# Kernel tuning notes

Hardware: AMD Instinct MI355X
Metric: run time of the kernel (lower is better)

Reference implementation:

```python
import jax, jax.numpy as jnp
import numpy as np

K = 3        # kernel size
STRIDE = 1
PAD = 1
DIL = 1


def setup_inputs() -> dict:
    key = jax.random.key(0)
    k1, k2, k3 = jax.random.split(key, 3)
    B, C, H, W, O = 4, 256, 64, 64, 256
    x = jax.random.normal(k1, (B, C, H, W), jnp.float32)
    # offset/mask predictor conv (kaiming-ish small init, zero bias per module init)
    w_off = jax.random.normal(k2, (3 * K * K, C, K, K), jnp.float32) * 0.01
    b_off = jnp.zeros((3 * K * K,), jnp.float32)
    # modulated deformable conv weight (bias=False)
    w_conv = jax.random.normal(k3, (O, C, K, K), jnp.float32) * 0.05
    return {"x": x, "w_off": w_off, "b_off": b_off, "w_conv": w_conv}


def _dfconv(x, w_off, b_off, w_conv):
    B, C, H, W = x.shape
    KK = K * K
    # 1) standard conv predicting offsets+mask: [B, 3*K*K, Ho, Wo]
    om = jax.lax.conv_general_dilated(
        x, w_off, (STRIDE, STRIDE), [(PAD, PAD), (PAD, PAD)],
        rhs_dilation=(DIL, DIL), dimension_numbers=("NCHW", "OIHW", "NCHW"))
    om = om + b_off[None, :, None, None]
    offset = om[:, : 2 * KK]                      # (dy,dx) interleaved per tap
    mask = jax.nn.sigmoid(om[:, 2 * KK:])         # [B, KK, Ho, Wo]
    Ho, Wo = offset.shape[-2:]
    off = offset.reshape(B, KK, 2, Ho, Wo)
    dy, dx = off[:, :, 0], off[:, :, 1]           # [B, KK, Ho, Wo]

    # 2) per-tap sampling coordinates in input space
    ky = jnp.repeat(jnp.arange(K), K).astype(x.dtype)   # tap row index [KK]
    kx = jnp.tile(jnp.arange(K), K).astype(x.dtype)     # tap col index [KK]
    base_y = (jnp.arange(Ho) * STRIDE - PAD).astype(x.dtype)
    base_x = (jnp.arange(Wo) * STRIDE - PAD).astype(x.dtype)
    py = dy + base_y[None, None, :, None] + (ky * DIL)[None, :, None, None]
    px = dx + base_x[None, None, None, :] + (kx * DIL)[None, :, None, None]

    # 3) bilinear sample with zero padding outside the image
    y0f = jnp.floor(py)
    x0f = jnp.floor(px)
    wy = py - y0f
    wx = px - x0f
    y0 = y0f.astype(jnp.int32)
    x0 = x0f.astype(jnp.int32)
    img = x.reshape(B, C, H * W)

    def gather(yi, xi):
        valid = ((yi >= 0) & (yi < H) & (xi >= 0) & (xi < W)).astype(x.dtype)
        idx = jnp.clip(yi, 0, H - 1) * W + jnp.clip(xi, 0, W - 1)
        g = jnp.take_along_axis(img, idx.reshape(B, 1, -1), axis=2)
        return g.reshape(B, C, KK, Ho, Wo) * valid[:, None]

    wy_ = wy[:, None]  # [B,1,KK,Ho,Wo]
    wx_ = wx[:, None]
    val = (gather(y0, x0) * (1 - wy_) * (1 - wx_)
           + gather(y0, x0 + 1) * (1 - wy_) * wx_
           + gather(y0 + 1, x0) * wy_ * (1 - wx_)
           + gather(y0 + 1, x0 + 1) * wy_ * wx_)

    # 4) modulation + weighted accumulation over taps and channels
    val = val * mask[:, None]                      # [B,C,KK,Ho,Wo]
    out = jnp.einsum("bckhw,ock->bohw", val, w_conv.reshape(w_conv.shape[0], C, KK))
    return out


def reference(x, w_off, b_off, w_conv):
    return _dfconv(x, w_off, b_off, w_conv)
```

## Files before the change

### kernel.cpp

```cpp
#include <hip/hip_runtime.h>
#include <hip/hip_bf16.h>

#define XH   64
#define XW   64
#define CIN  256
#define COUT 256
#define BATCH 4
#define KK9  9
#define M_TOT 16384
#define K_TOT 2304
#define NKSTEP 36

typedef __attribute__((ext_vector_type(8))) short short8;
typedef __attribute__((ext_vector_type(4))) float f32x4;

#define XT_OFF   0
#define XT_BYTES (BATCH*4096*CIN*2)
#define WT_OFF   (XT_OFF + XT_BYTES)
#define WT_BYTES (COUT*K_TOT*2)
#define WOT_OFF  (WT_OFF + WT_BYTES)
#define WOT_BYTES (36*2*2*64*8*2)

__device__ __forceinline__ float b2f(short s) {
  union { float f; unsigned u; } x;
  x.u = ((unsigned)(unsigned short)s) << 16;
  return x.f;
}

struct Taps { short8 t00, t01, t10, t11; };

__global__ __launch_bounds__(256) void k0_wt(const float* __restrict__ wconv,
                                             __hip_bfloat16* __restrict__ Wt3) {
  int e = blockIdx.x * 256 + threadIdx.x;
  int j3   = e & 7;
  int lane = (e >> 3) & 63;
  int kc   = (e >> 9) & 1;
  int og   = (e >> 10) & 15;
  int tk   = e >> 14;
  int o = og * 16 + (lane & 15);
  int k = tk * 64 + kc * 32 + ((lane >> 4) << 3) + j3;
  int kk = k >> 8, c = k & 255;
  float v = wconv[(o * CIN + c) * KK9 + kk];
  Wt3[e] = __float2bfloat16(v);
}

__global__ __launch_bounds__(256) void k0b_wot(const float* __restrict__ woff,
                                               __hip_bfloat16* __restrict__ Wot3) {
  int e = blockIdx.x * 256 + threadIdx.x;
  int j3   = e & 7;
  int lane = (e >> 3) & 63;
  int kc   = (e >> 9) & 1;
  int wc   = (e >> 10) & 1;
  int tk   = e >> 11;
  int oc = wc * 16 + (lane & 15);
  int k = tk * 64 + kc * 32 + ((lane >> 4) << 3) + j3;
  int kk = k >> 8, c = k & 255;
  float v = (oc < 27) ? woff[((size_t)(oc * 256 + c)) * 9 + kk] : 0.f;
  Wot3[e] = __float2bfloat16(v);
}

__global__ __launch_bounds__(256) void kt_xt(const float* __restrict__ x,
                                             __hip_bfloat16* __restrict__ xTh) {
  __shared__ float t[64][65];
  int blk = blockIdx.x;
  int hwg = blk & 63;
  int cg  = (blk >> 6) & 3;
  int b   = blk >> 8;
  int hw0 = hwg * 64, c0 = cg * 64;
  int l = threadIdx.x & 63, q = threadIdx.x >> 6;
  const float* xb = x + ((size_t)(b * 256 + c0) << 12) + hw0;
#pragma unroll
  for (int i = 0; i < 16; ++i) {
    int cl = q * 16 + i;
    t[cl][l] = xb[((size_t)cl << 12) + l];
  }
  __syncthreads();
  __hip_bfloat16* xTb = xTh + (((size_t)b << 12) + hw0) * 256 + c0;
#pragma unroll
  for (int i = 0; i < 16; ++i) {
    int hwl = q * 16 + i;
    xTb[(size_t)hwl * 256 + l] = __float2bfloat16(t[l][hwl]);
  }
}

__global__ __launch_bounds__(256, 2) void k23_fused(const __hip_bfloat16* __restrict__ xTh,
                                                    const __hip_bfloat16* __restrict__ Wt3,
                                                    const __hip_bfloat16* __restrict__ Wot3,
                                                    const float* __restrict__ boff,
                                                    float* __restrict__ out) {
  __shared__ __align__(16) __hip_bfloat16 sPV[2][32 * 64];
  __shared__ float sOM[32][33];
  __shared__ float sw00[288], sw01[288], sw10[288], sw11[288];
  __shared__ int   so00[288], so01[288], so10[288], so11[288];

  int bid = blockIdx.x;
  int tm = ((bid & 7) << 6) | (bid >> 3);
  int tid = threadIdx.x;
  int wv = tid >> 6, lane = tid & 63;
  int lo = lane & 15, hi = lane >> 4;
  int b = tm >> 7;
  int m0 = tm * 32;

  {
    int wr = wv >> 1, wc = wv & 1;
    int prow = tid >> 3;
    int pkb  = (tid & 7) * 8;
    int pcolz = pkb ^ ((prow & 7) << 3);
    int m_s = m0 + prow;
    int hw_s = m_s & 4095, h_s = hw_s >> 6, w_s = hw_s & 63;

    auto loadPatch = [&](int tkq) -> short8 {
      int kk = tkq >> 2, cc = tkq & 3;
      int ky = kk / 3, kx = kk - ky * 3;
      int yy = h_s + ky - 1, xx = w_s + kx - 1;
      short8 h8 = {0, 0, 0, 0, 0, 0, 0, 0};
      if (((unsigned)yy < 64u) && ((unsigned)xx < 64u))
        h8 = *(const short8*)(xTh + ((((size_t)b << 12) + yy * 64 + xx) << 8) + cc * 64 + pkb);
      return h8;
    };
    auto loadWot = [&](int tkq, short8 (&w2)[2]) {
#pragma unroll
      for (int kc = 0; kc < 2; ++kc)
        w2[kc] = *(const short8*)((const char*)Wot3
                  + ((((size_t)tkq * 2 + wc) * 2 + kc) << 10) + lane * 16);
    };

    f32x4 acc1 = {0.f, 0.f, 0.f, 0.f};
    short8 PA, PB, wUA[2], wUB[2];
    PA = loadPatch(0);
    loadWot(0, wUA);
    *(short8*)&sPV[0][prow * 64 + pcolz] = PA;
    PB = loadPatch(1);
    asm volatile("s_waitcnt lgkmcnt(0)" ::: "memory");
    __builtin_amdgcn_s_barrier();

    auto p1body = [&](int tk, short8& Puse, short8& Pload,
                      short8 (&wU)[2], short8 (&wL)[2]) {
      int cb = tk & 1, nb = cb ^ 1;
      loadWot(min(tk + 1, NKSTEP - 1), wL);
      Pload = loadPatch(min(tk + 2, NKSTEP - 1));
      __builtin_amdgcn_sched_barrier(0);
      *(short8*)&sPV[nb][prow * 64 + pcolz] = Puse;
#pragma unroll
      for (int kc = 0; kc < 2; ++kc) {
        int cz = (kc * 32 + hi * 8) ^ ((lo & 7) << 3);
        short8 bfr = *(const short8*)&sPV[cb][(wr * 16 + lo) * 64 + cz];
        acc1 = __builtin_amdgcn_mfma_f32_16x16x32_bf16(wU[kc], bfr, acc1, 0, 0, 0);
      }
      if (tk + 1 < NKSTEP) {
        asm volatile("s_waitcnt lgkmcnt(0)" ::: "memory");
        __builtin_amdgcn_s_barrier();
      }
    };
    for (int tkp = 0; tkp < NKSTEP; tkp += 2) {
      p1body(tkp,     PB, PA, wUA, wUB);
      p1body(tkp + 1, PA, PB, wUB, wUA);
    }

    int oc0 = wc * 16 + hi * 4;
#pragma unroll
    for (int r = 0; r < 4; ++r) {
      float bias = (oc0 + r < 27) ? boff[oc0 + r] : 0.f;
      sOM[wr * 16 + lo][oc0 + r] = acc1[r] + bias;
    }
  }
  __syncthreads();

  for (int it = tid; it < 288; it += 256) {
    int kk = it >> 5, row = it & 31;
    int m = m0 + row;
    int hw = m & 4095, h = hw >> 6, w = hw & 63;
    float dy = sOM[row][2 * kk];
    float dx = sOM[row][2 * kk + 1];
    float mz = sOM[row][18 + kk];
    int ky = kk / 3, kx = kk - ky * 3;
    float py = dy + (float)(h - 1 + ky);
    float px = dx + (float)(w - 1 + kx);
    float y0f = floorf(py), x0f = floorf(px);
    float wy = py - y0f, wx = px - x0f;
    int y0 = (int)y0f, x0 = (int)x0f;
    bool vy0 = (unsigned)y0 < 64u, vy1 = (unsigned)(y0 + 1) < 64u;
    bool vx0 = (unsigned)x0 < 64u, vx1 = (unsigned)(x0 + 1) < 64u;
    int cy0 = min(max(y0, 0), 63), cy1 = min(max(y0 + 1, 0), 63);
    int cx0 = min(max(x0, 0), 63), cx1 = min(max(x0 + 1, 0), 63);
    float mask = 1.f / (1.f + __expf(-mz));
    sw00[it] = (vy0 && vx0) ? (1.f - wy) * (1.f - wx) * mask : 0.f;
    sw01[it] = (vy0 && vx1) ? (1.f - wy) * wx * mask : 0.f;
    sw10[it] = (vy1 && vx0) ? wy * (1.f - wx) * mask : 0.f;
    sw11[it] = (vy1 && vx1) ? wy * wx * mask : 0.f;
    so00[it] = cy0 * 64 + cx0;
    so01[it] = cy0 * 64 + cx1;
    so10[it] = cy1 * 64 + cx0;
    so11[it] = cy1 * 64 + cx1;
  }
  __syncthreads();

  const __hip_bfloat16* xb = xTh + ((size_t)b << 20);
  int vrow = tid >> 3;
  int chq  = tid & 7;
  int colz = (chq * 8) ^ ((vrow & 7) << 3);

  auto loadTaps = [&](int tkq, Taps& T) {
    int it = (tkq >> 2) * 32 + vrow;
    const __hip_bfloat16* base = xb + (tkq & 3) * 64 + chq * 8;
    T.t00 = *(const short8*)(base + (size_t)so00[it] * 256);
    T.t01 = *(const short8*)(base + (size_t)so01[it] * 256);
    T.t10 = *(const short8*)(base + (size_t)so10[it] * 256);
    T.t11 = *(const short8*)(base + (size_t)so11[it] * 256);
  };
  auto buildV = [&](int tkq, const Taps& T, int buf) {
    int it = (tkq >> 2) * 32 + vrow;
    float a00 = sw00[it], a01 = sw01[it], a10 = sw10[it], a11 = sw11[it];
    __hip_bfloat16 h8[8];
#pragma unroll
    for (int j = 0; j < 8; ++j) {
      float v = a00 * b2f(T.t00[j]) + a01 * b2f(T.t01[j])
              + a10 * b2f(T.t10[j]) + a11 * b2f(T.t11[j]);
      h8[j] = __float2bfloat16(v);
    }
    *(short8*)&sPV[buf][vrow * 64 + colz] = *(const short8*)h8;
  };
  auto loadW = [&](int tkq, short8 (&aw)[8]) {
#pragma unroll
    for (int fo = 0; fo < 4; ++fo)
#pragma unroll
      for (int kc = 0; kc < 2; ++kc)
        aw[fo * 2 + kc] = *(const short8*)((const char*)Wt3
                          + ((((size_t)tkq * 16 + (wv * 4 + fo)) * 2 + kc) << 10)
                          + lane * 16);
  };

  f32x4 zero4 = {0.f, 0.f, 0.f, 0.f};
  f32x4 acc[4][2];
#pragma unroll
  for (int fo = 0; fo < 4; ++fo)
#pragma unroll
    for (int fm = 0; fm < 2; ++fm) acc[fo][fm] = zero4;

  Taps TA, TB;
  short8 awA[8], awB[8];
  loadW(0, awA);
  loadTaps(0, TA);
  buildV(0, TA, 0);
  loadTaps(1, TB);
  asm volatile("s_waitcnt lgkmcnt(0)" ::: "memory");
  __builtin_amdgcn_s_barrier();

  auto body = [&](int tk, Taps& Tuse, Taps& Tload,
                  short8 (&awUse)[8], short8 (&awLoad)[8]) {
    int cb = tk & 1, nb = cb ^ 1;
    loadW(min(tk + 1, NKSTEP - 1), awLoad);
    loadTaps(min(tk + 2, NKSTEP - 1), Tload);
    __builtin_amdgcn_sched_barrier(0);
    buildV(min(tk + 1, NKSTEP - 1), Tuse, nb);

    __builtin_amdgcn_s_setprio(1);
#pragma unroll
    for (int kc = 0; kc < 2; ++kc) {
      int cz = (kc * 32 + hi * 8) ^ ((lo & 7) << 3);
      short8 bv[2];
#pragma unroll
      for (int fm = 0; fm < 2; ++fm)
        bv[fm] = *(const short8*)&sPV[cb][(fm * 16 + lo) * 64 + cz];
#pragma unroll
      for (int fo = 0; fo < 4; ++fo)
#pragma unroll
        for (int fm = 0; fm < 2; ++fm)
          acc[fo][fm] = __builtin_amdgcn_mfma_f32_16x16x32_bf16(awUse[fo * 2 + kc], bv[fm], acc[fo][fm], 0, 0, 0);
    }
    __builtin_amdgcn_s_setprio(0);

    if (tk + 1 < NKSTEP) {
      asm volatile("s_waitcnt lgkmcnt(0)" ::: "memory");
      __builtin_amdgcn_s_barrier();
    }
  };

  for (int tkp = 0; tkp < NKSTEP; tkp += 2) {
    body(tkp,     TB, TA, awA, awB);
    body(tkp + 1, TA, TB, awB, awA);
  }

  int hwbase = m0 & 4095;
#pragma unroll
  for (int fo = 0; fo < 4; ++fo) {
    int o = wv * 64 + fo * 16 + hi * 4;
#pragma unroll
    for (int fm = 0; fm < 2; ++fm) {
      int mloc = hwbase + fm * 16 + lo;
#pragma unroll
      for (int r = 0; r < 4; ++r)
        out[((size_t)(b * 256 + o + r)) * 4096 + mloc] = acc[fo][fm][r];
    }
  }
}

extern "C" void kernel_launch(void* const* d_in, const int* in_sizes, int n_in,
                              void* d_out, int out_size, void* d_ws, size_t ws_size,
                              hipStream_t stream) {
  (void)in_sizes; (void)n_in; (void)out_size; (void)ws_size;
  const float* x     = (const float*)d_in[0];
  const float* woff  = (const float*)d_in[1];
  const float* boff  = (const float*)d_in[2];
  const float* wconv = (const float*)d_in[3];
  char* ws = (char*)d_ws;
  __hip_bfloat16* xTh  = (__hip_bfloat16*)(ws + XT_OFF);
  __hip_bfloat16* Wt3  = (__hip_bfloat16*)(ws + WT_OFF);
  __hip_bfloat16* Wot3 = (__hip_bfloat16*)(ws + WOT_OFF);
  float* out = (float*)d_out;

  hipLaunchKernelGGL(k0_wt,     dim3(2304), dim3(256), 0, stream, wconv, Wt3);
  hipLaunchKernelGGL(k0b_wot,   dim3(288),  dim3(256), 0, stream, woff, Wot3);
  hipLaunchKernelGGL(kt_xt,     dim3(1024), dim3(256), 0, stream, x, xTh);
  hipLaunchKernelGGL(k23_fused, dim3(512),  dim3(256), 0, stream, xTh, Wt3, Wot3, boff, out);
}
```

Before: 71.13 us.

## Double fused kernel block size to 512 threads with split-K offset conv

Raises the fused kernel from 256 to 512 threads per block, each wave now owning 32 output channels instead of 64. The offset-conv phase is split across two 256-thread groups, each reducing half of K into its own partial buffer; the partials and bias are summed afterwards. The main loop's gather switches to 4-element loads per thread. This is meant to raise occupancy and spread the gather and MFMA work over more waves. The cost is that the offset-conv loop loses its software pipelining and now issues two full barriers per step.

```diff
diff --git a/kernel.cpp b/kernel.cpp
--- a/kernel.cpp
+++ b/kernel.cpp
@@ -10,8 +10,10 @@
 #define M_TOT 16384
 #define K_TOT 2304
 #define NKSTEP 36
+#define HKSTEP 18
 
 typedef __attribute__((ext_vector_type(8))) short short8;
+typedef __attribute__((ext_vector_type(4))) short short4v;
 typedef __attribute__((ext_vector_type(4))) float f32x4;
 
 #define XT_OFF   0
@@ -27,7 +29,7 @@
   return x.f;
 }
 
-struct Taps { short8 t00, t01, t10, t11; };
+struct Taps4 { short4v t00, t01, t10, t11; };
 
 __global__ __launch_bounds__(256) void k0_wt(const float* __restrict__ wconv,
                                              __hip_bfloat16* __restrict__ Wt3) {
@@ -83,13 +85,13 @@
   }
 }
 
-__global__ __launch_bounds__(256, 2) void k23_fused(const __hip_bfloat16* __restrict__ xTh,
+__global__ __launch_bounds__(512, 4) void k23_fused(const __hip_bfloat16* __restrict__ xTh,
                                                     const __hip_bfloat16* __restrict__ Wt3,
                                                     const __hip_bfloat16* __restrict__ Wot3,
                                                     const float* __restrict__ boff,
                                                     float* __restrict__ out) {
   __shared__ __align__(16) __hip_bfloat16 sPV[2][32 * 64];
-  __shared__ float sOM[32][33];
+  __shared__ float sOMp[2][32][33];
   __shared__ float sw00[288], sw01[288], sw10[288], sw11[288];
   __shared__ int   so00[288], so01[288], so10[288], so11[288];
 
@@ -102,77 +104,51 @@
   int m0 = tm * 32;
 
   {
-    int wr = wv >> 1, wc = wv & 1;
-    int prow = tid >> 3;
-    int pkb  = (tid & 7) * 8;
+    int g  = wv >> 2;
+    int wq = wv & 3;
+    int wr = wq >> 1, wc = wq & 1;
+    int gt = tid & 255;
+    int prow = gt >> 3;
+    int pkb  = (gt & 7) * 8;
     int pcolz = pkb ^ ((prow & 7) << 3);
     int m_s = m0 + prow;
     int hw_s = m_s & 4095, h_s = hw_s >> 6, w_s = hw_s & 63;
 
-    auto loadPatch = [&](int tkq) -> short8 {
-      int kk = tkq >> 2, cc = tkq & 3;
+    f32x4 acc1 = {0.f, 0.f, 0.f, 0.f};
+    for (int s = 0; s < HKSTEP; ++s) {
+      int tk = g * HKSTEP + s;
+      int kk = tk >> 2, cc = tk & 3;
       int ky = kk / 3, kx = kk - ky * 3;
       int yy = h_s + ky - 1, xx = w_s + kx - 1;
       short8 h8 = {0, 0, 0, 0, 0, 0, 0, 0};
       if (((unsigned)yy < 64u) && ((unsigned)xx < 64u))
         h8 = *(const short8*)(xTh + ((((size_t)b << 12) + yy * 64 + xx) << 8) + cc * 64 + pkb);
-      return h8;
-    };
-    auto loadWot = [&](int tkq, short8 (&w2)[2]) {
-#pragma unroll
-      for (int kc = 0; kc < 2; ++kc)
-        w2[kc] = *(const short8*)((const char*)Wot3
-                  + ((((size_t)tkq * 2 + wc) * 2 + kc) << 10) + lane * 16);
-    };
-
-    f32x4 acc1 = {0.f, 0.f, 0.f, 0.f};
-    short8 PA, PB, wUA[2], wUB[2];
-    PA = loadPatch(0);
-    loadWot(0, wUA);
-    *(short8*)&sPV[0][prow * 64 + pcolz] = PA;
-    PB = loadPatch(1);
-    asm volatile("s_waitcnt lgkmcnt(0)" ::: "memory");
-    __builtin_amdgcn_s_barrier();
-
-    auto p1body = [&](int tk, short8& Puse, short8& Pload,
-                      short8 (&wU)[2], short8 (&wL)[2]) {
-      int cb = tk & 1, nb = cb ^ 1;
-      loadWot(min(tk + 1, NKSTEP - 1), wL);
-      Pload = loadPatch(min(tk + 2, NKSTEP - 1));
-      __builtin_amdgcn_sched_barrier(0);
-      *(short8*)&sPV[nb][prow * 64 + pcolz] = Puse;
+      *(short8*)&sPV[g][prow * 64 + pcolz] = h8;
+      __syncthreads();
 #pragma unroll
       for (int kc = 0; kc < 2; ++kc) {
         int cz = (kc * 32 + hi * 8) ^ ((lo & 7) << 3);
-        short8 bfr = *(const short8*)&sPV[cb][(wr * 16 + lo) * 64 + cz];
-        acc1 = __builtin_amdgcn_mfma_f32_16x16x32_bf16(wU[kc], bfr, acc1, 0, 0, 0);
+        short8 bfr = *(const short8*)&sPV[g][(wr * 16 + lo) * 64 + cz];
+        short8 a = *(const short8*)((const char*)Wot3
+                    + ((((size_t)tk * 2 + wc) * 2 + kc) << 10) + lane * 16);
+        acc1 = __builtin_amdgcn_mfma_f32_16x16x32_bf16(a, bfr, acc1, 0, 0, 0);
       }
-      if (tk + 1 < NKSTEP) {
-        asm volatile("s_waitcnt lgkmcnt(0)" ::: "memory");
-        __builtin_amdgcn_s_barrier();
-      }
-    };
-    for (int tkp = 0; tkp < NKSTEP; tkp += 2) {
-      p1body(tkp,     PB, PA, wUA, wUB);
-      p1body(tkp + 1, PA, PB, wUB, wUA);
-    }
-
+      __syncthreads();
+    }
     int oc0 = wc * 16 + hi * 4;
 #pragma unroll
-    for (int r = 0; r < 4; ++r) {
-      float bias = (oc0 + r < 27) ? boff[oc0 + r] : 0.f;
-      sOM[wr * 16 + lo][oc0 + r] = acc1[r] + bias;
-    }
+    for (int r = 0; r < 4; ++r)
+      sOMp[g][wr * 16 + lo][oc0 + r] = acc1[r];
   }
   __syncthreads();
 
-  for (int it = tid; it < 288; it += 256) {
+  for (int it = tid; it < 288; it += 512) {
     int kk = it >> 5, row = it & 31;
     int m = m0 + row;
     int hw = m & 4095, h = hw >> 6, w = hw & 63;
-    float dy = sOM[row][2 * kk];
-    float dx = sOM[row][2 * kk + 1];
-    float mz = sOM[row][18 + kk];
+    float dy = sOMp[0][row][2 * kk]     + sOMp[1][row][2 * kk]     + boff[2 * kk];
+    float dx = sOMp[0][row][2 * kk + 1] + sOMp[1][row][2 * kk + 1] + boff[2 * kk + 1];
+    float mz = sOMp[0][row][18 + kk]    + sOMp[1][row][18 + kk]    + boff[18 + kk];
     int ky = kk / 3, kx = kk - ky * 3;
     float py = dy + (float)(h - 1 + ky);
     float px = dx + (float)(w - 1 + kx);
@@ -196,49 +172,49 @@
   __syncthreads();
 
   const __hip_bfloat16* xb = xTh + ((size_t)b << 20);
-  int vrow = tid >> 3;
-  int chq  = tid & 7;
-  int colz = (chq * 8) ^ ((vrow & 7) << 3);
-
-  auto loadTaps = [&](int tkq, Taps& T) {
+  int vrow = tid >> 4;
+  int chq  = tid & 15;
+  int colz = (chq * 4) ^ ((vrow & 7) << 3);
+
+  auto loadTaps = [&](int tkq, Taps4& T) {
     int it = (tkq >> 2) * 32 + vrow;
-    const __hip_bfloat16* base = xb + (tkq & 3) * 64 + chq * 8;
-    T.t00 = *(const short8*)(base + (size_t)so00[it] * 256);
-    T.t01 = *(const short8*)(base + (size_t)so01[it] * 256);
-    T.t10 = *(const short8*)(base + (size_t)so10[it] * 256);
-    T.t11 = *(const short8*)(base + (size_t)so11[it] * 256);
-  };
-  auto buildV = [&](int tkq, const Taps& T, int buf) {
+    const __hip_bfloat16* base = xb + (tkq & 3) * 64 + chq * 4;
+    T.t00 = *(const short4v*)(base + (size_t)so00[it] * 256);
+    T.t01 = *(const short4v*)(base + (size_t)so01[it] * 256);
+    T.t10 = *(const short4v*)(base + (size_t)so10[it] * 256);
+    T.t11 = *(const short4v*)(base + (size_t)so11[it] * 256);
+  };
+  auto buildV = [&](int tkq, const Taps4& T, int buf) {
     int it = (tkq >> 2) * 32 + vrow;
     float a00 = sw00[it], a01 = sw01[it], a10 = sw10[it], a11 = sw11[it];
-    __hip_bfloat16 h8[8];
-#pragma unroll
-    for (int j = 0; j < 8; ++j) {
+    __hip_bfloat16 h4[4];
+#pragma unroll
+    for (int j = 0; j < 4; ++j) {
       float v = a00 * b2f(T.t00[j]) + a01 * b2f(T.t01[j])
               + a10 * b2f(T.t10[j]) + a11 * b2f(T.t11[j]);
-      h8[j] = __float2bfloat16(v);
-    }
-    *(short8*)&sPV[buf][vrow * 64 + colz] = *(const short8*)h8;
-  };
-  auto loadW = [&](int tkq, short8 (&aw)[8]) {
-#pragma unroll
-    for (int fo = 0; fo < 4; ++fo)
+      h4[j] = __float2bfloat16(v);
+    }
+    *(short4v*)&sPV[buf][vrow * 64 + colz] = *(const short4v*)h4;
+  };
+  auto loadW = [&](int tkq, short8 (&aw)[4]) {
+#pragma unroll
+    for (int fo = 0; fo < 2; ++fo)
 #pragma unroll
       for (int kc = 0; kc < 2; ++kc)
         aw[fo * 2 + kc] = *(const short8*)((const char*)Wt3
-                          + ((((size_t)tkq * 16 + (wv * 4 + fo)) * 2 + kc) << 10)
+                          + ((((size_t)tkq * 16 + (wv * 2 + fo)) * 2 + kc) << 10)
                           + lane * 16);
   };
 
   f32x4 zero4 = {0.f, 0.f, 0.f, 0.f};
-  f32x4 acc[4][2];
-#pragma unroll
-  for (int fo = 0; fo < 4; ++fo)
+  f32x4 acc[2][2];
+#pragma unroll
+  for (int fo = 0; fo < 2; ++fo)
 #pragma unroll
     for (int fm = 0; fm < 2; ++fm) acc[fo][fm] = zero4;
 
-  Taps TA, TB;
-  short8 awA[8], awB[8];
+  Taps4 TA, TB;
+  short8 awA[4], awB[4];
   loadW(0, awA);
   loadTaps(0, TA);
   buildV(0, TA, 0);
@@ -246,13 +222,14 @@
   asm volatile("s_waitcnt lgkmcnt(0)" ::: "memory");
   __builtin_amdgcn_s_barrier();
 
-  auto body = [&](int tk, Taps& Tuse, Taps& Tload,
-                  short8 (&awUse)[8], short8 (&awLoad)[8]) {
+  auto body = [&](int tk, Taps4& Tuse, Taps4& Tload,
+                  short8 (&awUse)[4], short8 (&awLoad)[4]) {
     int cb = tk & 1, nb = cb ^ 1;
-    loadW(min(tk + 1, NKSTEP - 1), awLoad);
-    loadTaps(min(tk + 2, NKSTEP - 1), Tload);
+    int tk1 = min(tk + 1, NKSTEP - 1), tk2 = min(tk + 2, NKSTEP - 1);
+    loadW(tk1, awLoad);
+    loadTaps(tk2, Tload);
     __builtin_amdgcn_sched_barrier(0);
-    buildV(min(tk + 1, NKSTEP - 1), Tuse, nb);
+    buildV(tk1, Tuse, nb);
 
     __builtin_amdgcn_s_setprio(1);
 #pragma unroll
@@ -263,7 +240,7 @@
       for (int fm = 0; fm < 2; ++fm)
         bv[fm] = *(const short8*)&sPV[cb][(fm * 16 + lo) * 64 + cz];
 #pragma unroll
-      for (int fo = 0; fo < 4; ++fo)
+      for (int fo = 0; fo < 2; ++fo)
 #pragma unroll
         for (int fm = 0; fm < 2; ++fm)
           acc[fo][fm] = __builtin_amdgcn_mfma_f32_16x16x32_bf16(awUse[fo * 2 + kc], bv[fm], acc[fo][fm], 0, 0, 0);
@@ -283,8 +260,8 @@
 
   int hwbase = m0 & 4095;
 #pragma unroll
-  for (int fo = 0; fo < 4; ++fo) {
-    int o = wv * 64 + fo * 16 + hi * 4;
+  for (int fo = 0; fo < 2; ++fo) {
+    int o = wv * 32 + fo * 16 + hi * 4;
 #pragma unroll
     for (int fm = 0; fm < 2; ++fm) {
       int mloc = hwbase + fm * 16 + lo;
@@ -312,5 +289,5 @@
   hipLaunchKernelGGL(k0_wt,     dim3(2304), dim3(256), 0, stream, wconv, Wt3);
   hipLaunchKernelGGL(k0b_wot,   dim3(288),  dim3(256), 0, stream, woff, Wot3);
   hipLaunchKernelGGL(kt_xt,     dim3(1024), dim3(256), 0, stream, x, xTh);
-  hipLaunchKernelGGL(k23_fused, dim3(512),  dim3(256), 0, stream, xTh, Wt3, Wot3, boff, out);
-}
+  hipLaunchKernelGGL(k23_fused, dim3(512),  dim3(512), 0, stream, xTh, Wt3, Wot3, boff, out);
+}
```

Result: slower. 72.94 us (+2.5%).

## Restructure offset-conv phase to load whole tap into four LDS buffers per barrier

Applied to the files above, without the earlier changes.

The offset-predictor GEMM phase now loops over the 9 taps and loads all four 64-channel chunks of the patch into four LDS buffers at once, with two block barriers per tap. It replaces the per-k-step double-buffered, register-prefetched pipeline. This cuts barrier count from 36 to 18 steps and lets the loads for a tap issue together. The cost is that the prefetch overlap between loads and MFMA is lost and more LDS is used, which could lower occupancy. The weight fragments are now loaded inline rather than prefetched.

```diff
diff --git a/kernel.cpp b/kernel.cpp
--- a/kernel.cpp
+++ b/kernel.cpp
@@ -88,10 +88,12 @@
                                                     const __hip_bfloat16* __restrict__ Wot3,
                                                     const float* __restrict__ boff,
                                                     float* __restrict__ out) {
-  __shared__ __align__(16) __hip_bfloat16 sPV[2][32 * 64];
+  __shared__ __align__(16) __hip_bfloat16 sPatch[4][32 * 64];
   __shared__ float sOM[32][33];
   __shared__ float sw00[288], sw01[288], sw10[288], sw11[288];
   __shared__ int   so00[288], so01[288], so10[288], so11[288];
+
+  __hip_bfloat16 (*sPV)[32 * 64] = sPatch;
 
   int bid = blockIdx.x;
   int tm = ((bid & 7) << 6) | (bid >> 3);
@@ -109,52 +111,34 @@
     int m_s = m0 + prow;
     int hw_s = m_s & 4095, h_s = hw_s >> 6, w_s = hw_s & 63;
 
-    auto loadPatch = [&](int tkq) -> short8 {
-      int kk = tkq >> 2, cc = tkq & 3;
+    f32x4 acc1 = {0.f, 0.f, 0.f, 0.f};
+    const short8 zero8 = {0,0,0,0,0,0,0,0};
+
+    for (int kk = 0; kk < KK9; ++kk) {
       int ky = kk / 3, kx = kk - ky * 3;
       int yy = h_s + ky - 1, xx = w_s + kx - 1;
-      short8 h8 = {0, 0, 0, 0, 0, 0, 0, 0};
-      if (((unsigned)yy < 64u) && ((unsigned)xx < 64u))
-        h8 = *(const short8*)(xTh + ((((size_t)b << 12) + yy * 64 + xx) << 8) + cc * 64 + pkb);
-      return h8;
-    };
-    auto loadWot = [&](int tkq, short8 (&w2)[2]) {
-#pragma unroll
-      for (int kc = 0; kc < 2; ++kc)
-        w2[kc] = *(const short8*)((const char*)Wot3
-                  + ((((size_t)tkq * 2 + wc) * 2 + kc) << 10) + lane * 16);
-    };
-
-    f32x4 acc1 = {0.f, 0.f, 0.f, 0.f};
-    short8 PA, PB, wUA[2], wUB[2];
-    PA = loadPatch(0);
-    loadWot(0, wUA);
-    *(short8*)&sPV[0][prow * 64 + pcolz] = PA;
-    PB = loadPatch(1);
-    asm volatile("s_waitcnt lgkmcnt(0)" ::: "memory");
-    __builtin_amdgcn_s_barrier();
-
-    auto p1body = [&](int tk, short8& Puse, short8& Pload,
-                      short8 (&wU)[2], short8 (&wL)[2]) {
-      int cb = tk & 1, nb = cb ^ 1;
-      loadWot(min(tk + 1, NKSTEP - 1), wL);
-      Pload = loadPatch(min(tk + 2, NKSTEP - 1));
-      __builtin_amdgcn_sched_barrier(0);
-      *(short8*)&sPV[nb][prow * 64 + pcolz] = Puse;
-#pragma unroll
-      for (int kc = 0; kc < 2; ++kc) {
-        int cz = (kc * 32 + hi * 8) ^ ((lo & 7) << 3);
-        short8 bfr = *(const short8*)&sPV[cb][(wr * 16 + lo) * 64 + cz];
-        acc1 = __builtin_amdgcn_mfma_f32_16x16x32_bf16(wU[kc], bfr, acc1, 0, 0, 0);
+      bool valid = ((unsigned)yy < 64u) && ((unsigned)xx < 64u);
+      int cy = min(max(yy, 0), 63), cx = min(max(xx, 0), 63);
+      const __hip_bfloat16* src = xTh + ((((size_t)b << 12) + cy * 64 + cx) << 8) + pkb;
+#pragma unroll
+      for (int cc = 0; cc < 4; ++cc) {
+        short8 h8 = valid ? *(const short8*)(src + cc * 64) : zero8;
+        *(short8*)&sPatch[cc][prow * 64 + pcolz] = h8;
       }
-      if (tk + 1 < NKSTEP) {
-        asm volatile("s_waitcnt lgkmcnt(0)" ::: "memory");
-        __builtin_amdgcn_s_barrier();
+      __syncthreads();
+#pragma unroll
+      for (int cc = 0; cc < 4; ++cc) {
+        int tk = kk * 4 + cc;
+#pragma unroll
+        for (int kc = 0; kc < 2; ++kc) {
+          int cz = (kc * 32 + hi * 8) ^ ((lo & 7) << 3);
+          short8 bfr = *(const short8*)&sPatch[cc][(wr * 16 + lo) * 64 + cz];
+          short8 a = *(const short8*)((const char*)Wot3
+                      + ((((size_t)tk * 2 + wc) * 2 + kc) << 10) + lane * 16);
+          acc1 = __builtin_amdgcn_mfma_f32_16x16x32_bf16(a, bfr, acc1, 0, 0, 0);
+        }
       }
-    };
-    for (int tkp = 0; tkp < NKSTEP; tkp += 2) {
-      p1body(tkp,     PB, PA, wUA, wUB);
-      p1body(tkp + 1, PA, PB, wUB, wUA);
+      __syncthreads();
     }
 
     int oc0 = wc * 16 + hi * 4;
@@ -249,10 +233,11 @@
   auto body = [&](int tk, Taps& Tuse, Taps& Tload,
                   short8 (&awUse)[8], short8 (&awLoad)[8]) {
     int cb = tk & 1, nb = cb ^ 1;
-    loadW(min(tk + 1, NKSTEP - 1), awLoad);
-    loadTaps(min(tk + 2, NKSTEP - 1), Tload);
+    int tk1 = min(tk + 1, NKSTEP - 1), tk2 = min(tk + 2, NKSTEP - 1);
+    loadW(tk1, awLoad);
+    loadTaps(tk2, Tload);
     __builtin_amdgcn_sched_barrier(0);
-    buildV(min(tk + 1, NKSTEP - 1), Tuse, nb);
+    buildV(tk1, Tuse, nb);
 
     __builtin_amdgcn_s_setprio(1);
 #pragma unroll
```

Result: faster. 67.99 us (-4.4%).
